# Optimization experiments

Hardware: AMD Instinct MI355X
Metric: run time of the kernel (lower is better)

## Reference

```python
import jax, jax.numpy as jnp
import numpy as np

N_NODES = 50000
N_EDGES = 600000
DIN, DH, DOUT = 128, 256, 128
BN_EPS = 1e-5
LRELU_SLOPE = 0.01


def setup_inputs() -> dict:
    key = jax.random.key(0)
    ks = jax.random.split(key, 16)
    rn = lambda k, s, sc=0.05: jax.random.normal(k, s, dtype=jnp.float32) * sc
    return {
        'nodes': jax.random.normal(ks[0], (N_NODES, DIN), dtype=jnp.float32),
        'src': jax.random.randint(ks[1], (N_EDGES,), 0, N_NODES, dtype=jnp.int32),
        'dst': jax.random.randint(ks[2], (N_EDGES,), 0, N_NODES, dtype=jnp.int32),
        # FeedForward params
        'Wf1': rn(ks[3], (DIN, DH)), 'bf1': jnp.zeros((DH,), jnp.float32),
        'gf1': jnp.ones((DH,), jnp.float32), 'bef1': jnp.zeros((DH,), jnp.float32),
        'Wf2': rn(ks[4], (DH, DIN)), 'bf2': jnp.zeros((DIN,), jnp.float32),
        'gf2': jnp.ones((DIN,), jnp.float32), 'bef2': jnp.zeros((DIN,), jnp.float32),
        # SAGEConv 1 (in->hidden)
        'Ws1': rn(ks[5], (DIN, DH)), 'Wn1': rn(ks[6], (DIN, DH)), 'b1': jnp.zeros((DH,), jnp.float32),
        'gs1': jnp.ones((DH,), jnp.float32), 'bs1': jnp.zeros((DH,), jnp.float32),
        # SAGEConv 2 (hidden->out)
        'Ws2': rn(ks[7], (DH, DOUT)), 'Wn2': rn(ks[8], (DH, DOUT)), 'b2': jnp.zeros((DOUT,), jnp.float32),
        'gs2': jnp.ones((DOUT,), jnp.float32), 'bs2': jnp.zeros((DOUT,), jnp.float32),
    }


def _bn(x, gamma, beta):
    # BatchNorm1d, training mode: batch stats over node dim, biased variance
    mu = jnp.mean(x, axis=0)
    var = jnp.mean(jnp.square(x - mu), axis=0)
    return (x - mu) * jax.lax.rsqrt(var + BN_EPS) * gamma + beta


def _sage_mean(x, src, dst, Wself, Wneigh, bias):
    # DGL SAGEConv('mean'): out = x@Wself + mean_{src->dst}(x[src])@Wneigh + bias
    n = x.shape[0]
    deg = jax.ops.segment_sum(jnp.ones_like(src, dtype=x.dtype), dst, num_segments=n)
    agg = jax.ops.segment_sum(x[src], dst, num_segments=n)  # [N, d] irregular scatter-add
    h_neigh = agg / jnp.maximum(deg, 1.0)[:, None]
    return x @ Wself + h_neigh @ Wneigh + bias


def reference(nodes, src, dst, Wf1, bf1, gf1, bef1, Wf2, bf2, gf2, bef2,
              Ws1, Wn1, b1, gs1, bs1, Ws2, Wn2, b2, gs2, bs2):
    # FeedForward (dropout=0 -> identity)
    h = jax.nn.relu(_bn(nodes @ Wf1 + bf1, gf1, bef1))
    h = jax.nn.relu(_bn(h @ Wf2 + bf2, gf2, bef2))
    # SAGE layer 1
    h1 = _sage_mean(h, src, dst, Ws1, Wn1, b1)
    h1 = jax.nn.leaky_relu(_bn(h1, gs1, bs1), LRELU_SLOPE)
    # SAGE layer 2
    h2 = _sage_mean(h1, src, dst, Ws2, Wn2, b2)
    return jax.nn.leaky_relu(_bn(h2, gs2, bs2), LRELU_SLOPE)
```

## Files before the change

### kernel.cpp

```cpp
#include <hip/hip_runtime.h>

#define DIN 128
#define BN_EPS 1e-5f

typedef __attribute__((ext_vector_type(8))) short bf16x8;
typedef __attribute__((ext_vector_type(4))) float f32x4;
typedef unsigned int u32;

__device__ __forceinline__ ushort f2bf(float f) {
    unsigned u = __float_as_uint(f);
    u += 0x7fffu + ((u >> 16) & 1u);
    return (ushort)(u >> 16);
}
__device__ __forceinline__ float bf2f(ushort h) {
    return __uint_as_float(((unsigned)h) << 16);
}

template<int KC, int STATS>
__global__ __launch_bounds__(256) void gemm_wreg(
    const ushort* __restrict__ A, const ushort* __restrict__ BT,
    ushort* __restrict__ C, int mStrips, int N, int K, int logNG,
    float* __restrict__ gsums, float* __restrict__ gsqs)
{
    int tid = threadIdx.x;
    int lane = tid & 63;
    int gw = blockIdx.x * 4 + (tid >> 6);
    int wg = gw & ((1 << logNG) - 1);
    int set = gw >> logNG;
    int totalSets = (gridDim.x * 4) >> logNG;
    int cl = lane & 15, q = lane >> 4;
    int colBase = wg * 64;

    bf16x8 bf[4][KC];
    #pragma unroll
    for (int nt = 0; nt < 4; nt++) {
        const ushort* bp = BT + (long)(colBase + nt * 16 + cl) * K + q * 8;
        #pragma unroll
        for (int kc = 0; kc < KC; kc++)
            bf[nt][kc] = *(const bf16x8*)(bp + kc * 32);
    }

    float ssum[4] = {0.f, 0.f, 0.f, 0.f};
    float ssq[4]  = {0.f, 0.f, 0.f, 0.f};

    for (int strip = set; strip < mStrips; strip += totalSets) {
        int rowBase = strip * 16;
        const ushort* ap = A + (long)(rowBase + cl) * K + q * 8;
        bf16x8 af[KC];
        #pragma unroll
        for (int kc = 0; kc < KC; kc++)
            af[kc] = *(const bf16x8*)(ap + kc * 32);
        f32x4 acc[4] = {};
        #pragma unroll
        for (int kc = 0; kc < KC; kc++)
            #pragma unroll
            for (int nt = 0; nt < 4; nt++)
                acc[nt] = __builtin_amdgcn_mfma_f32_16x16x32_bf16(af[kc], bf[nt][kc], acc[nt], 0, 0, 0);
        #pragma unroll
        for (int nt = 0; nt < 4; nt++) {
            #pragma unroll
            for (int r = 0; r < 4; r++) {
                float v = acc[nt][r];
                long row = rowBase + q * 4 + r;
                C[row * N + colBase + nt * 16 + cl] = f2bf(v);
                if (STATS) { ssum[nt] += v; ssq[nt] += v * v; }
            }
        }
    }

    if (STATS) {
        #pragma unroll
        for (int nt = 0; nt < 4; nt++) {
            ssum[nt] += __shfl_xor(ssum[nt], 16, 64);
            ssum[nt] += __shfl_xor(ssum[nt], 32, 64);
            ssq[nt]  += __shfl_xor(ssq[nt], 16, 64);
            ssq[nt]  += __shfl_xor(ssq[nt], 32, 64);
        }
        if (q == 0) {
            #pragma unroll
            for (int nt = 0; nt < 4; nt++) {
                atomicAdd(&gsums[colBase + nt * 16 + cl], ssum[nt]);
                atomicAdd(&gsqs[colBase + nt * 16 + cl], ssq[nt]);
            }
        }
    }
}

__global__ void bnparam_kernel(const float* __restrict__ sums, const float* __restrict__ sqs,
                               const float* __restrict__ gamma, const float* __restrict__ beta,
                               float* __restrict__ scale, float* __restrict__ shift,
                               int N, float invM)
{
    int c = blockIdx.x * blockDim.x + threadIdx.x;
    if (c < N) {
        float mean = sums[c] * invM;
        float var = sqs[c] * invM - mean * mean;
        float sc = gamma[c] * rsqrtf(var + BN_EPS);
        scale[c] = sc;
        shift[c] = beta[c] - mean * sc;
    }
}

__global__ __launch_bounds__(256) void bnact_bf16(
    const ushort* __restrict__ X, const float* __restrict__ scale, const float* __restrict__ shift,
    ushort* __restrict__ O, int total4, int logN, int outStride, float negSlope)
{
    int stride = gridDim.x * blockDim.x;
    int Nm1 = (1 << logN) - 1;
    for (int t = blockIdx.x * blockDim.x + threadIdx.x; t < total4; t += stride) {
        int idx = t * 4;
        int row = idx >> logN;
        int c = idx & Nm1;
        ushort4 v4 = *(const ushort4*)&X[idx];
        float4 sc = *(const float4*)&scale[c];
        float4 sh = *(const float4*)&shift[c];
        float a = bf2f(v4.x) * sc.x + sh.x; a = (a > 0.f) ? a : a * negSlope;
        float b = bf2f(v4.y) * sc.y + sh.y; b = (b > 0.f) ? b : b * negSlope;
        float d = bf2f(v4.z) * sc.z + sh.z; d = (d > 0.f) ? d : d * negSlope;
        float e = bf2f(v4.w) * sc.w + sh.w; e = (e > 0.f) ? e : e * negSlope;
        ushort4 o; o.x = f2bf(a); o.y = f2bf(b); o.z = f2bf(d); o.w = f2bf(e);
        *(ushort4*)&O[(long)row * outStride + c] = o;
    }
}

__global__ __launch_bounds__(256) void bnact_f32(
    float* __restrict__ X, const float* __restrict__ scale, const float* __restrict__ shift,
    int total4, int logN, float negSlope)
{
    int stride = gridDim.x * blockDim.x;
    int Nm1 = (1 << logN) - 1;
    for (int t = blockIdx.x * blockDim.x + threadIdx.x; t < total4; t += stride) {
        int idx = t * 4;
        int c = idx & Nm1;
        float4 v = *(const float4*)&X[idx];
        float4 sc = *(const float4*)&scale[c];
        float4 sh = *(const float4*)&shift[c];
        float a = v.x * sc.x + sh.x; a = (a > 0.f) ? a : a * negSlope;
        float b = v.y * sc.y + sh.y; b = (b > 0.f) ? b : b * negSlope;
        float d = v.z * sc.z + sh.z; d = (d > 0.f) ? d : d * negSlope;
        float e = v.w * sc.w + sh.w; e = (e > 0.f) ? e : e * negSlope;
        *(float4*)&X[idx] = make_float4(a, b, d, e);
    }
}

__global__ __launch_bounds__(256) void colstats128(
    const float* __restrict__ X, float* __restrict__ sums, float* __restrict__ sqs, int M)
{
    __shared__ float ss[128], sq[128];
    int tid = threadIdx.x;
    if (tid < 128) { ss[tid] = 0.f; sq[tid] = 0.f; }
    __syncthreads();
    int cg = tid & 31;
    int worker = (blockIdx.x << 3) | (tid >> 5);
    int totalW = gridDim.x << 3;
    float4 s4 = make_float4(0, 0, 0, 0), q4 = make_float4(0, 0, 0, 0);
    for (int r = worker; r < M; r += totalW) {
        float4 v = *(const float4*)&X[(long)r * 128 + cg * 4];
        s4.x += v.x; s4.y += v.y; s4.z += v.z; s4.w += v.w;
        q4.x += v.x * v.x; q4.y += v.y * v.y; q4.z += v.z * v.z; q4.w += v.w * v.w;
    }
    atomicAdd(&ss[cg * 4 + 0], s4.x); atomicAdd(&sq[cg * 4 + 0], q4.x);
    atomicAdd(&ss[cg * 4 + 1], s4.y); atomicAdd(&sq[cg * 4 + 1], q4.y);
    atomicAdd(&ss[cg * 4 + 2], s4.z); atomicAdd(&sq[cg * 4 + 2], q4.z);
    atomicAdd(&ss[cg * 4 + 3], s4.w); atomicAdd(&sq[cg * 4 + 3], q4.w);
    __syncthreads();
    if (tid < 128) { atomicAdd(&sums[tid], ss[tid]); atomicAdd(&sqs[tid], sq[tid]); }
}

__global__ void convert_nodes(const float* __restrict__ X, ushort* __restrict__ O, int total4)
{
    int t = blockIdx.x * blockDim.x + threadIdx.x;
    if (t < total4) {
        float4 v = *(const float4*)&X[t * 4];
        ushort4 o; o.x = f2bf(v.x); o.y = f2bf(v.y); o.z = f2bf(v.z); o.w = f2bf(v.w);
        *(ushort4*)&O[t * 4] = o;
    }
}

__global__ void wt_all(const float* __restrict__ W0, const float* __restrict__ W1,
                       const float* __restrict__ W2, const float* __restrict__ W3,
                       const float* __restrict__ W4, const float* __restrict__ W5,
                       ushort* __restrict__ WT)
{
    int seg = blockIdx.y;
    const float* W; int logK, dstBase, stride, kOff;
    switch (seg) {
        case 0: W = W0; logK = 7; dstBase = 0;      stride = 128; kOff = 0;   break;
        case 1: W = W1; logK = 8; dstBase = 32768;  stride = 256; kOff = 0;   break;
        case 2: W = W2; logK = 7; dstBase = 65536;  stride = 256; kOff = 0;   break;
        case 3: W = W3; logK = 7; dstBase = 65536;  stride = 256; kOff = 128; break;
        case 4: W = W4; logK = 8; dstBase = 131072; stride = 256; kOff = 0;   break;
        default:W = W5; logK = 8; dstBase = 163840; stride = 256; kOff = 0;   break;
    }
    int t = blockIdx.x * blockDim.x + threadIdx.x;
    int N = 32768 >> logK;
    int k = t & ((1 << logK) - 1);
    int n = t >> logK;
    WT[(long)dstBase + (long)n * stride + kOff + k] = f2bf(W[(long)k * N + n]);
}

__global__ void degcount_kernel(const int* __restrict__ dst, int* __restrict__ degi, int E)
{
    int i = blockIdx.x * blockDim.x + threadIdx.x;
    if (i < E) atomicAdd(&degi[dst[i]], 1);
}

__global__ __launch_bounds__(256) void scan_block_sums(const int* __restrict__ degi,
                                                       int* __restrict__ partial, int n)
{
    __shared__ int s[256];
    int i = blockIdx.x * 256 + threadIdx.x;
    s[threadIdx.x] = (i < n) ? degi[i] : 0;
    __syncthreads();
    for (int off = 128; off > 0; off >>= 1) {
        if (threadIdx.x < off) s[threadIdx.x] += s[threadIdx.x + off];
        __syncthreads();
    }
    if (threadIdx.x == 0) partial[blockIdx.x] = s[0];
}

__global__ __launch_bounds__(256) void scan_partials(int* __restrict__ partial, int nb)
{
    __shared__ int s[256];
    int v = (threadIdx.x < nb) ? partial[threadIdx.x] : 0;
    s[threadIdx.x] = v;
    __syncthreads();
    for (int off = 1; off < 256; off <<= 1) {
        int t = (threadIdx.x >= off) ? s[threadIdx.x - off] : 0;
        __syncthreads();
        s[threadIdx.x] += t;
        __syncthreads();
    }
    if (threadIdx.x < nb) partial[threadIdx.x] = s[threadIdx.x] - v;
}

__global__ __launch_bounds__(256) void scan_final(const int* __restrict__ degi,
                                                  const int* __restrict__ partial,
                                                  int* __restrict__ rowstart, int n)
{
    __shared__ int s[256];
    int i = blockIdx.x * 256 + threadIdx.x;
    int v = (i < n) ? degi[i] : 0;
    s[threadIdx.x] = v;
    __syncthreads();
    for (int off = 1; off < 256; off <<= 1) {
        int t = (threadIdx.x >= off) ? s[threadIdx.x - off] : 0;
        __syncthreads();
        s[threadIdx.x] += t;
        __syncthreads();
    }
    if (i < n) rowstart[i] = partial[blockIdx.x] + s[threadIdx.x] - v;
}

__global__ void fillcsr_kernel(const int* __restrict__ src, const int* __restrict__ dst,
                               const int* __restrict__ rowstart, int* __restrict__ cursor,
                               int* __restrict__ csr, int E)
{
    int i = blockIdx.x * blockDim.x + threadIdx.x;
    if (i < E) {
        int d = dst[i];
        int p = atomicAdd(&cursor[d], 1);
        csr[rowstart[d] + p] = src[i];
    }
}

__global__ __launch_bounds__(256) void gather_bf(
    const ushort* __restrict__ X, const int* __restrict__ rowstart,
    const int* __restrict__ degi, const int* __restrict__ csr,
    ushort* __restrict__ O, int nN)
{
    int wv = (blockIdx.x * blockDim.x + threadIdx.x) >> 6;
    int lane = threadIdx.x & 63;
    if (wv >= nN) return;
    int start = rowstart[wv], d = degi[wv];
    float a0 = 0.f, a1 = 0.f;
    int col = lane * 2;
    int j = 0;
    for (; j + 4 <= d; j += 4) {
        int s0 = csr[start + j + 0];
        int s1 = csr[start + j + 1];
        int s2 = csr[start + j + 2];
        int s3 = csr[start + j + 3];
        unsigned p0 = *(const unsigned*)(X + (long)s0 * 256 + col);
        unsigned p1 = *(const unsigned*)(X + (long)s1 * 256 + col);
        unsigned p2 = *(const unsigned*)(X + (long)s2 * 256 + col);
        unsigned p3 = *(const unsigned*)(X + (long)s3 * 256 + col);
        a0 += bf2f((ushort)(p0 & 0xffff)) + bf2f((ushort)(p1 & 0xffff))
            + bf2f((ushort)(p2 & 0xffff)) + bf2f((ushort)(p3 & 0xffff));
        a1 += bf2f((ushort)(p0 >> 16)) + bf2f((ushort)(p1 >> 16))
            + bf2f((ushort)(p2 >> 16)) + bf2f((ushort)(p3 >> 16));
    }
    for (; j < d; j++) {
        int s0 = csr[start + j];
        unsigned p0 = *(const unsigned*)(X + (long)s0 * 256 + col);
        a0 += bf2f((ushort)(p0 & 0xffff));
        a1 += bf2f((ushort)(p0 >> 16));
    }
    float inv = 1.f / fmaxf((float)d, 1.f);
    unsigned o = (unsigned)f2bf(a0 * inv) | ((unsigned)f2bf(a1 * inv) << 16);
    *(unsigned*)(O + (long)wv * 256 + col) = o;
}

__global__ __launch_bounds__(256) void gather_fuse(
    const ushort* __restrict__ Z, const int* __restrict__ rowstart,
    const int* __restrict__ degi, const int* __restrict__ csr,
    float* __restrict__ O, int nN)
{
    int wv = (blockIdx.x * blockDim.x + threadIdx.x) >> 6;
    int lane = threadIdx.x & 63;
    if (wv >= nN) return;
    int start = rowstart[wv], d = degi[wv];
    float a0 = 0.f, a1 = 0.f;
    int col = lane * 2;
    int j = 0;
    for (; j + 4 <= d; j += 4) {
        int s0 = csr[start + j + 0];
        int s1 = csr[start + j + 1];
        int s2 = csr[start + j + 2];
        int s3 = csr[start + j + 3];
        unsigned p0 = *(const unsigned*)(Z + (long)s0 * 256 + col);
        unsigned p1 = *(const unsigned*)(Z + (long)s1 * 256 + col);
        unsigned p2 = *(const unsigned*)(Z + (long)s2 * 256 + col);
        unsigned p3 = *(const unsigned*)(Z + (long)s3 * 256 + col);
        a0 += bf2f((ushort)(p0 & 0xffff)) + bf2f((ushort)(p1 & 0xffff))
            + bf2f((ushort)(p2 & 0xffff)) + bf2f((ushort)(p3 & 0xffff));
        a1 += bf2f((ushort)(p0 >> 16)) + bf2f((ushort)(p1 >> 16))
            + bf2f((ushort)(p2 >> 16)) + bf2f((ushort)(p3 >> 16));
    }
    for (; j < d; j++) {
        int s0 = csr[start + j];
        unsigned p0 = *(const unsigned*)(Z + (long)s0 * 256 + col);
        a0 += bf2f((ushort)(p0 & 0xffff));
        a1 += bf2f((ushort)(p0 >> 16));
    }
    float inv = 1.f / fmaxf((float)d, 1.f);
    unsigned sv = *(const unsigned*)(Z + (long)wv * 256 + 128 + col);
    float s0 = bf2f((ushort)(sv & 0xffff));
    float s1 = bf2f((ushort)(sv >> 16));
    *(float2*)(O + (long)wv * 128 + col) = make_float2(a0 * inv + s0, a1 * inv + s1);
}

extern "C" void kernel_launch(void* const* d_in, const int* in_sizes, int n_in,
                              void* d_out, int out_size, void* d_ws, size_t ws_size,
                              hipStream_t stream)
{
    const float* nodes = (const float*)d_in[0];
    const int*   src   = (const int*)d_in[1];
    const int*   dst   = (const int*)d_in[2];
    const float* Wf1   = (const float*)d_in[3];
    const float* gf1   = (const float*)d_in[5];
    const float* bef1  = (const float*)d_in[6];
    const float* Wf2   = (const float*)d_in[7];
    const float* gf2   = (const float*)d_in[9];
    const float* bef2  = (const float*)d_in[10];
    const float* Ws1   = (const float*)d_in[11];
    const float* Wn1   = (const float*)d_in[12];
    const float* gs1   = (const float*)d_in[14];
    const float* bs1   = (const float*)d_in[15];
    const float* Ws2   = (const float*)d_in[16];
    const float* Wn2   = (const float*)d_in[17];
    const float* gs2   = (const float*)d_in[19];
    const float* bs2   = (const float*)d_in[20];

    int nN = in_sizes[0] / DIN;
    int nE = in_sizes[1];
    float* out = (float*)d_out;
    int mStrips = nN / 16;

    ushort* PRE = (ushort*)d_ws;
    ushort* BF1 = PRE + (size_t)nN * 256;
    ushort* BF2 = BF1 + (size_t)nN * 256;
    float* stats = (float*)(BF2 + (size_t)nN * 256);
    float* scale = stats + 2048;
    float* shift = scale + 256;
    ushort* WT   = (ushort*)(shift + 256);
    int* degi     = (int*)(WT + 196608);
    int* cursor   = degi + nN;
    int* rowstart = cursor + nN;
    int* partial  = rowstart + nN;
    int* csr      = partial + 256;

    ushort* Wf1T = WT;
    ushort* Wf2T = WT + 32768;
    ushort* Wc1T = WT + 65536;
    ushort* Wc2T = WT + 131072;

    dim3 blk(256);
    auto cdiv = [](int a, int b) { return (a + b - 1) / b; };
    int nScanBlocks = cdiv(nN, 256);

    convert_nodes<<<dim3(cdiv(nN * DIN / 4, 256)), blk, 0, stream>>>(nodes, BF1, nN * DIN / 4);
    wt_all<<<dim3(128, 6), blk, 0, stream>>>(Wf1, Wf2, Ws1, Wn1, Wn2, Ws2, WT);
    hipMemsetAsync(stats, 0, 2048 * sizeof(float), stream);
    hipMemsetAsync(degi, 0, 2 * (size_t)nN * sizeof(int), stream);

    degcount_kernel<<<dim3(cdiv(nE, 256)), blk, 0, stream>>>(dst, degi, nE);
    scan_block_sums<<<dim3(nScanBlocks), blk, 0, stream>>>(degi, partial, nN);
    scan_partials<<<dim3(1), blk, 0, stream>>>(partial, nScanBlocks);
    scan_final<<<dim3(nScanBlocks), blk, 0, stream>>>(degi, partial, rowstart, nN);
    fillcsr_kernel<<<dim3(cdiv(nE, 256)), blk, 0, stream>>>(src, dst, rowstart, cursor, csr, nE);

    gemm_wreg<4, 1><<<dim3(512), blk, 0, stream>>>(BF1, Wf1T, PRE, mStrips, 256, 128, 2, stats, stats + 256);
    bnparam_kernel<<<dim3(1), blk, 0, stream>>>(stats, stats + 256, gf1, bef1, scale, shift, 256, 1.0f / nN);
    bnact_bf16<<<dim3(2048), blk, 0, stream>>>(PRE, scale, shift, BF1, nN * 256 / 4, 8, 256, 0.0f);

    gemm_wreg<8, 1><<<dim3(256), blk, 0, stream>>>(BF1, Wf2T, PRE, mStrips, 128, 256, 1, stats + 512, stats + 768);
    bnparam_kernel<<<dim3(1), blk, 0, stream>>>(stats + 512, stats + 768, gf2, bef2, scale, shift, 128, 1.0f / nN);
    bnact_bf16<<<dim3(2048), blk, 0, stream>>>(PRE, scale, shift, BF2, nN * 128 / 4, 7, 256, 0.0f);

    gather_bf<<<dim3(cdiv(nN * 64, 256)), blk, 0, stream>>>(BF2, rowstart, degi, csr, BF2 + 128, nN);

    gemm_wreg<8, 1><<<dim3(512), blk, 0, stream>>>(BF2, Wc1T, PRE, mStrips, 256, 256, 2, stats + 1024, stats + 1280);
    bnparam_kernel<<<dim3(1), blk, 0, stream>>>(stats + 1024, stats + 1280, gs1, bs1, scale, shift, 256, 1.0f / nN);
    bnact_bf16<<<dim3(2048), blk, 0, stream>>>(PRE, scale, shift, BF1, nN * 256 / 4, 8, 256, 0.01f);

    gemm_wreg<8, 0><<<dim3(512), blk, 0, stream>>>(BF1, Wc2T, BF2, mStrips, 256, 256, 2, nullptr, nullptr);
    gather_fuse<<<dim3(cdiv(nN * 64, 256)), blk, 0, stream>>>(BF2, rowstart, degi, csr, out, nN);

    colstats128<<<dim3(120), blk, 0, stream>>>(out, stats + 1536, stats + 1792, nN);
    bnparam_kernel<<<dim3(1), blk, 0, stream>>>(stats + 1536, stats + 1792, gs2, bs2, scale, shift, 128, 1.0f / nN);
    bnact_f32<<<dim3(2048), blk, 0, stream>>>(out, scale, shift, nN * 128 / 4, 7, 0.01f);
}
```

Measured before the change: 418.5 us.

## Fuse setup kernels, BN parameter computation, scan stages, and final column stats

Merges the input conversion, weight transposes and memsets into one setup kernel. BN scale/shift computation moves into each bnact kernel's prologue, the partial-sum scan is folded into scan_final, and the final column statistics are accumulated inside gather_fuse instead of a separate pass. bnact kernels also switch to 8-wide vector loads. The aim is to cut launch count and one full read of the output, at the cost of redundant per-block BN parameter and prefix recomputation plus more atomics.

```diff
diff --git a/kernel.cpp b/kernel.cpp
--- a/kernel.cpp
+++ b/kernel.cpp
@@ -4,8 +4,8 @@
 #define BN_EPS 1e-5f
 
 typedef __attribute__((ext_vector_type(8))) short bf16x8;
+typedef __attribute__((ext_vector_type(8))) unsigned short us8;
 typedef __attribute__((ext_vector_type(4))) float f32x4;
-typedef unsigned int u32;
 
 __device__ __forceinline__ ushort f2bf(float f) {
     unsigned u = __float_as_uint(f);
@@ -86,117 +86,128 @@
     }
 }
 
-__global__ void bnparam_kernel(const float* __restrict__ sums, const float* __restrict__ sqs,
-                               const float* __restrict__ gamma, const float* __restrict__ beta,
-                               float* __restrict__ scale, float* __restrict__ shift,
-                               int N, float invM)
-{
-    int c = blockIdx.x * blockDim.x + threadIdx.x;
-    if (c < N) {
-        float mean = sums[c] * invM;
-        float var = sqs[c] * invM - mean * mean;
-        float sc = gamma[c] * rsqrtf(var + BN_EPS);
-        scale[c] = sc;
-        shift[c] = beta[c] - mean * sc;
-    }
-}
-
+__global__ __launch_bounds__(256) void setup_all(
+    const float* __restrict__ nodes, ushort* __restrict__ Xbf, int nConv4, int nbConv,
+    const float* __restrict__ W0, const float* __restrict__ W1,
+    const float* __restrict__ W2, const float* __restrict__ W3,
+    const float* __restrict__ W4, const float* __restrict__ W5,
+    ushort* __restrict__ WT,
+    int* __restrict__ zeroInts, int nZero4, int nbZero,
+    float* __restrict__ stats)
+{
+    int b = blockIdx.x;
+    int tid = threadIdx.x;
+    if (b < nbConv) {
+        int t = b * 256 + tid;
+        if (t < nConv4) {
+            float4 v = *(const float4*)&nodes[(long)t * 4];
+            ushort4 o; o.x = f2bf(v.x); o.y = f2bf(v.y); o.z = f2bf(v.z); o.w = f2bf(v.w);
+            *(ushort4*)&Xbf[(long)t * 4] = o;
+        }
+        return;
+    }
+    b -= nbConv;
+    if (b < 768) {
+        int seg = b >> 7;
+        const float* W; int logK, dstBase, stride, kOff;
+        switch (seg) {
+            case 0: W = W0; logK = 7; dstBase = 0;      stride = 128; kOff = 0;   break;
+            case 1: W = W1; logK = 8; dstBase = 32768;  stride = 256; kOff = 0;   break;
+            case 2: W = W2; logK = 7; dstBase = 65536;  stride = 256; kOff = 0;   break;
+            case 3: W = W3; logK = 7; dstBase = 65536;  stride = 256; kOff = 128; break;
+            case 4: W = W4; logK = 8; dstBase = 131072; stride = 256; kOff = 0;   break;
+            default:W = W5; logK = 8; dstBase = 163840; stride = 256; kOff = 0;   break;
+        }
+        int t = (b & 127) * 256 + tid;
+        int N = 32768 >> logK;
+        int k = t & ((1 << logK) - 1);
+        int n = t >> logK;
+        WT[(long)dstBase + (long)n * stride + kOff + k] = f2bf(W[(long)k * N + n]);
+        return;
+    }
+    b -= 768;
+    if (b < nbZero) {
+        int t = b * 256 + tid;
+        if (t < nZero4) *(int4*)&zeroInts[(long)t * 4] = make_int4(0, 0, 0, 0);
+        return;
+    }
+    b -= nbZero;
+    int t = b * 256 + tid;
+    if (t < 512) *(float4*)&stats[(long)t * 4] = make_float4(0, 0, 0, 0);
+}
+
+template<int LOGN>
 __global__ __launch_bounds__(256) void bnact_bf16(
-    const ushort* __restrict__ X, const float* __restrict__ scale, const float* __restrict__ shift,
-    ushort* __restrict__ O, int total4, int logN, int outStride, float negSlope)
-{
-    int stride = gridDim.x * blockDim.x;
-    int Nm1 = (1 << logN) - 1;
-    for (int t = blockIdx.x * blockDim.x + threadIdx.x; t < total4; t += stride) {
-        int idx = t * 4;
-        int row = idx >> logN;
-        int c = idx & Nm1;
-        ushort4 v4 = *(const ushort4*)&X[idx];
-        float4 sc = *(const float4*)&scale[c];
-        float4 sh = *(const float4*)&shift[c];
-        float a = bf2f(v4.x) * sc.x + sh.x; a = (a > 0.f) ? a : a * negSlope;
-        float b = bf2f(v4.y) * sc.y + sh.y; b = (b > 0.f) ? b : b * negSlope;
-        float d = bf2f(v4.z) * sc.z + sh.z; d = (d > 0.f) ? d : d * negSlope;
-        float e = bf2f(v4.w) * sc.w + sh.w; e = (e > 0.f) ? e : e * negSlope;
-        ushort4 o; o.x = f2bf(a); o.y = f2bf(b); o.z = f2bf(d); o.w = f2bf(e);
-        *(ushort4*)&O[(long)row * outStride + c] = o;
+    const ushort* __restrict__ X,
+    const float* __restrict__ sums, const float* __restrict__ sqs,
+    const float* __restrict__ gamma, const float* __restrict__ beta, float invM,
+    ushort* __restrict__ O, int nRows, int outStride, float negSlope)
+{
+    constexpr int NCH = 1 << LOGN;
+    __shared__ float ssc[NCH], ssh[NCH];
+    int tid = threadIdx.x;
+    if (tid < NCH) {
+        float mean = sums[tid] * invM;
+        float var = sqs[tid] * invM - mean * mean;
+        float sc = gamma[tid] * rsqrtf(var + BN_EPS);
+        ssc[tid] = sc;
+        ssh[tid] = beta[tid] - mean * sc;
+    }
+    __syncthreads();
+    int cb = (tid * 8) & (NCH - 1);
+    float4 sA = *(const float4*)&ssc[cb];
+    float4 sB = *(const float4*)&ssc[cb + 4];
+    float4 hA = *(const float4*)&ssh[cb];
+    float4 hB = *(const float4*)&ssh[cb + 4];
+    const int rpb = (256 * 8) >> LOGN;
+    int r0 = blockIdx.x * rpb + ((tid * 8) >> LOGN);
+    int rstride = gridDim.x * rpb;
+    for (int row = r0; row < nRows; row += rstride) {
+        us8 v = *(const us8*)&X[(long)row * NCH + cb];
+        float f0 = bf2f(v[0]) * sA.x + hA.x; f0 = (f0 > 0.f) ? f0 : f0 * negSlope;
+        float f1 = bf2f(v[1]) * sA.y + hA.y; f1 = (f1 > 0.f) ? f1 : f1 * negSlope;
+        float f2 = bf2f(v[2]) * sA.z + hA.z; f2 = (f2 > 0.f) ? f2 : f2 * negSlope;
+        float f3 = bf2f(v[3]) * sA.w + hA.w; f3 = (f3 > 0.f) ? f3 : f3 * negSlope;
+        float f4 = bf2f(v[4]) * sB.x + hB.x; f4 = (f4 > 0.f) ? f4 : f4 * negSlope;
+        float f5 = bf2f(v[5]) * sB.y + hB.y; f5 = (f5 > 0.f) ? f5 : f5 * negSlope;
+        float f6 = bf2f(v[6]) * sB.z + hB.z; f6 = (f6 > 0.f) ? f6 : f6 * negSlope;
+        float f7 = bf2f(v[7]) * sB.w + hB.w; f7 = (f7 > 0.f) ? f7 : f7 * negSlope;
+        us8 o;
+        o[0] = f2bf(f0); o[1] = f2bf(f1); o[2] = f2bf(f2); o[3] = f2bf(f3);
+        o[4] = f2bf(f4); o[5] = f2bf(f5); o[6] = f2bf(f6); o[7] = f2bf(f7);
+        *(us8*)&O[(long)row * outStride + cb] = o;
     }
 }
 
 __global__ __launch_bounds__(256) void bnact_f32(
-    float* __restrict__ X, const float* __restrict__ scale, const float* __restrict__ shift,
-    int total4, int logN, float negSlope)
-{
-    int stride = gridDim.x * blockDim.x;
-    int Nm1 = (1 << logN) - 1;
-    for (int t = blockIdx.x * blockDim.x + threadIdx.x; t < total4; t += stride) {
-        int idx = t * 4;
-        int c = idx & Nm1;
-        float4 v = *(const float4*)&X[idx];
-        float4 sc = *(const float4*)&scale[c];
-        float4 sh = *(const float4*)&shift[c];
+    float* __restrict__ X,
+    const float* __restrict__ sums, const float* __restrict__ sqs,
+    const float* __restrict__ gamma, const float* __restrict__ beta, float invM,
+    int nRows, float negSlope)
+{
+    __shared__ float ssc[128], ssh[128];
+    int tid = threadIdx.x;
+    if (tid < 128) {
+        float mean = sums[tid] * invM;
+        float var = sqs[tid] * invM - mean * mean;
+        float sc = gamma[tid] * rsqrtf(var + BN_EPS);
+        ssc[tid] = sc;
+        ssh[tid] = beta[tid] - mean * sc;
+    }
+    __syncthreads();
+    int cb = (tid * 4) & 127;
+    float4 sc = *(const float4*)&ssc[cb];
+    float4 sh = *(const float4*)&ssh[cb];
+    int r0 = blockIdx.x * 8 + ((tid * 4) >> 7);
+    int rstride = gridDim.x * 8;
+    for (int row = r0; row < nRows; row += rstride) {
+        float4 v = *(const float4*)&X[(long)row * 128 + cb];
         float a = v.x * sc.x + sh.x; a = (a > 0.f) ? a : a * negSlope;
         float b = v.y * sc.y + sh.y; b = (b > 0.f) ? b : b * negSlope;
         float d = v.z * sc.z + sh.z; d = (d > 0.f) ? d : d * negSlope;
         float e = v.w * sc.w + sh.w; e = (e > 0.f) ? e : e * negSlope;
-        *(float4*)&X[idx] = make_float4(a, b, d, e);
-    }
-}
-
-__global__ __launch_bounds__(256) void colstats128(
-    const float* __restrict__ X, float* __restrict__ sums, float* __restrict__ sqs, int M)
-{
-    __shared__ float ss[128], sq[128];
-    int tid = threadIdx.x;
-    if (tid < 128) { ss[tid] = 0.f; sq[tid] = 0.f; }
-    __syncthreads();
-    int cg = tid & 31;
-    int worker = (blockIdx.x << 3) | (tid >> 5);
-    int totalW = gridDim.x << 3;
-    float4 s4 = make_float4(0, 0, 0, 0), q4 = make_float4(0, 0, 0, 0);
-    for (int r = worker; r < M; r += totalW) {
-        float4 v = *(const float4*)&X[(long)r * 128 + cg * 4];
-        s4.x += v.x; s4.y += v.y; s4.z += v.z; s4.w += v.w;
-        q4.x += v.x * v.x; q4.y += v.y * v.y; q4.z += v.z * v.z; q4.w += v.w * v.w;
-    }
-    atomicAdd(&ss[cg * 4 + 0], s4.x); atomicAdd(&sq[cg * 4 + 0], q4.x);
-    atomicAdd(&ss[cg * 4 + 1], s4.y); atomicAdd(&sq[cg * 4 + 1], q4.y);
-    atomicAdd(&ss[cg * 4 + 2], s4.z); atomicAdd(&sq[cg * 4 + 2], q4.z);
-    atomicAdd(&ss[cg * 4 + 3], s4.w); atomicAdd(&sq[cg * 4 + 3], q4.w);
-    __syncthreads();
-    if (tid < 128) { atomicAdd(&sums[tid], ss[tid]); atomicAdd(&sqs[tid], sq[tid]); }
-}
-
-__global__ void convert_nodes(const float* __restrict__ X, ushort* __restrict__ O, int total4)
-{
-    int t = blockIdx.x * blockDim.x + threadIdx.x;
-    if (t < total4) {
-        float4 v = *(const float4*)&X[t * 4];
-        ushort4 o; o.x = f2bf(v.x); o.y = f2bf(v.y); o.z = f2bf(v.z); o.w = f2bf(v.w);
-        *(ushort4*)&O[t * 4] = o;
-    }
-}
-
-__global__ void wt_all(const float* __restrict__ W0, const float* __restrict__ W1,
-                       const float* __restrict__ W2, const float* __restrict__ W3,
-                       const float* __restrict__ W4, const float* __restrict__ W5,
-                       ushort* __restrict__ WT)
-{
-    int seg = blockIdx.y;
-    const float* W; int logK, dstBase, stride, kOff;
-    switch (seg) {
-        case 0: W = W0; logK = 7; dstBase = 0;      stride = 128; kOff = 0;   break;
-        case 1: W = W1; logK = 8; dstBase = 32768;  stride = 256; kOff = 0;   break;
-        case 2: W = W2; logK = 7; dstBase = 65536;  stride = 256; kOff = 0;   break;
-        case 3: W = W3; logK = 7; dstBase = 65536;  stride = 256; kOff = 128; break;
-        case 4: W = W4; logK = 8; dstBase = 131072; stride = 256; kOff = 0;   break;
-        default:W = W5; logK = 8; dstBase = 163840; stride = 256; kOff = 0;   break;
-    }
-    int t = blockIdx.x * blockDim.x + threadIdx.x;
-    int N = 32768 >> logK;
-    int k = t & ((1 << logK) - 1);
-    int n = t >> logK;
-    WT[(long)dstBase + (long)n * stride + kOff + k] = f2bf(W[(long)k * N + n]);
+        *(float4*)&X[(long)row * 128 + cb] = make_float4(a, b, d, e);
+    }
 }
 
 __global__ void degcount_kernel(const int* __restrict__ dst, int* __restrict__ degi, int E)
@@ -219,37 +230,31 @@
     if (threadIdx.x == 0) partial[blockIdx.x] = s[0];
 }
 
-__global__ __launch_bounds__(256) void scan_partials(int* __restrict__ partial, int nb)
-{
-    __shared__ int s[256];
-    int v = (threadIdx.x < nb) ? partial[threadIdx.x] : 0;
-    s[threadIdx.x] = v;
-    __syncthreads();
-    for (int off = 1; off < 256; off <<= 1) {
-        int t = (threadIdx.x >= off) ? s[threadIdx.x - off] : 0;
-        __syncthreads();
-        s[threadIdx.x] += t;
-        __syncthreads();
-    }
-    if (threadIdx.x < nb) partial[threadIdx.x] = s[threadIdx.x] - v;
-}
-
 __global__ __launch_bounds__(256) void scan_final(const int* __restrict__ degi,
                                                   const int* __restrict__ partial,
-                                                  int* __restrict__ rowstart, int n)
+                                                  int* __restrict__ rowstart, int n, int nb)
 {
     __shared__ int s[256];
-    int i = blockIdx.x * 256 + threadIdx.x;
+    __shared__ int ps[256];
+    int tid = threadIdx.x;
+    ps[tid] = (tid < nb && tid < (int)blockIdx.x) ? partial[tid] : 0;
+    __syncthreads();
+    for (int off = 128; off > 0; off >>= 1) {
+        if (tid < off) ps[tid] += ps[tid + off];
+        __syncthreads();
+    }
+    int offset = ps[0];
+    int i = blockIdx.x * 256 + tid;
     int v = (i < n) ? degi[i] : 0;
-    s[threadIdx.x] = v;
+    s[tid] = v;
     __syncthreads();
     for (int off = 1; off < 256; off <<= 1) {
-        int t = (threadIdx.x >= off) ? s[threadIdx.x - off] : 0;
+        int t = (tid >= off) ? s[tid - off] : 0;
         __syncthreads();
-        s[threadIdx.x] += t;
+        s[tid] += t;
         __syncthreads();
     }
-    if (i < n) rowstart[i] = partial[blockIdx.x] + s[threadIdx.x] - v;
+    if (i < n) rowstart[i] = offset + s[tid] - v;
 }
 
 __global__ void fillcsr_kernel(const int* __restrict__ src, const int* __restrict__ dst,
@@ -304,40 +309,52 @@
 __global__ __launch_bounds__(256) void gather_fuse(
     const ushort* __restrict__ Z, const int* __restrict__ rowstart,
     const int* __restrict__ degi, const int* __restrict__ csr,
-    float* __restrict__ O, int nN)
-{
-    int wv = (blockIdx.x * blockDim.x + threadIdx.x) >> 6;
-    int lane = threadIdx.x & 63;
-    if (wv >= nN) return;
-    int start = rowstart[wv], d = degi[wv];
-    float a0 = 0.f, a1 = 0.f;
+    float* __restrict__ O, float* __restrict__ gsums, float* __restrict__ gsqs, int nN)
+{
+    __shared__ float ls[128], lq[128];
+    int tid = threadIdx.x;
+    if (tid < 128) { ls[tid] = 0.f; lq[tid] = 0.f; }
+    __syncthreads();
+    int lane = tid & 63;
     int col = lane * 2;
-    int j = 0;
-    for (; j + 4 <= d; j += 4) {
-        int s0 = csr[start + j + 0];
-        int s1 = csr[start + j + 1];
-        int s2 = csr[start + j + 2];
-        int s3 = csr[start + j + 3];
-        unsigned p0 = *(const unsigned*)(Z + (long)s0 * 256 + col);
-        unsigned p1 = *(const unsigned*)(Z + (long)s1 * 256 + col);
-        unsigned p2 = *(const unsigned*)(Z + (long)s2 * 256 + col);
-        unsigned p3 = *(const unsigned*)(Z + (long)s3 * 256 + col);
-        a0 += bf2f((ushort)(p0 & 0xffff)) + bf2f((ushort)(p1 & 0xffff))
-            + bf2f((ushort)(p2 & 0xffff)) + bf2f((ushort)(p3 & 0xffff));
-        a1 += bf2f((ushort)(p0 >> 16)) + bf2f((ushort)(p1 >> 16))
-            + bf2f((ushort)(p2 >> 16)) + bf2f((ushort)(p3 >> 16));
-    }
-    for (; j < d; j++) {
-        int s0 = csr[start + j];
-        unsigned p0 = *(const unsigned*)(Z + (long)s0 * 256 + col);
-        a0 += bf2f((ushort)(p0 & 0xffff));
-        a1 += bf2f((ushort)(p0 >> 16));
-    }
-    float inv = 1.f / fmaxf((float)d, 1.f);
-    unsigned sv = *(const unsigned*)(Z + (long)wv * 256 + 128 + col);
-    float s0 = bf2f((ushort)(sv & 0xffff));
-    float s1 = bf2f((ushort)(sv >> 16));
-    *(float2*)(O + (long)wv * 128 + col) = make_float2(a0 * inv + s0, a1 * inv + s1);
+    float sum0 = 0.f, sq0 = 0.f, sum1 = 0.f, sq1 = 0.f;
+    int wstride = gridDim.x * 4;
+    for (int wv = blockIdx.x * 4 + (tid >> 6); wv < nN; wv += wstride) {
+        int start = rowstart[wv], d = degi[wv];
+        float a0 = 0.f, a1 = 0.f;
+        int j = 0;
+        for (; j + 4 <= d; j += 4) {
+            int s0 = csr[start + j + 0];
+            int s1 = csr[start + j + 1];
+            int s2 = csr[start + j + 2];
+            int s3 = csr[start + j + 3];
+            unsigned p0 = *(const unsigned*)(Z + (long)s0 * 256 + col);
+            unsigned p1 = *(const unsigned*)(Z + (long)s1 * 256 + col);
+            unsigned p2 = *(const unsigned*)(Z + (long)s2 * 256 + col);
+            unsigned p3 = *(const unsigned*)(Z + (long)s3 * 256 + col);
+            a0 += bf2f((ushort)(p0 & 0xffff)) + bf2f((ushort)(p1 & 0xffff))
+                + bf2f((ushort)(p2 & 0xffff)) + bf2f((ushort)(p3 & 0xffff));
+            a1 += bf2f((ushort)(p0 >> 16)) + bf2f((ushort)(p1 >> 16))
+                + bf2f((ushort)(p2 >> 16)) + bf2f((ushort)(p3 >> 16));
+        }
+        for (; j < d; j++) {
+            int s0 = csr[start + j];
+            unsigned p0 = *(const unsigned*)(Z + (long)s0 * 256 + col);
+            a0 += bf2f((ushort)(p0 & 0xffff));
+            a1 += bf2f((ushort)(p0 >> 16));
+        }
+        float inv = 1.f / fmaxf((float)d, 1.f);
+        unsigned sv = *(const unsigned*)(Z + (long)wv * 256 + 128 + col);
+        float r0 = a0 * inv + bf2f((ushort)(sv & 0xffff));
+        float r1 = a1 * inv + bf2f((ushort)(sv >> 16));
+        *(float2*)(O + (long)wv * 128 + col) = make_float2(r0, r1);
+        sum0 += r0; sq0 += r0 * r0;
+        sum1 += r1; sq1 += r1 * r1;
+    }
+    atomicAdd(&ls[col], sum0);     atomicAdd(&lq[col], sq0);
+    atomicAdd(&ls[col + 1], sum1); atomicAdd(&lq[col + 1], sq1);
+    __syncthreads();
+    if (tid < 128) { atomicAdd(&gsums[tid], ls[tid]); atomicAdd(&gsqs[tid], lq[tid]); }
 }
 
 extern "C" void kernel_launch(void* const* d_in, const int* in_sizes, int n_in,
@@ -366,6 +383,7 @@
     int nE = in_sizes[1];
     float* out = (float*)d_out;
     int mStrips = nN / 16;
+    float invM = 1.0f / nN;
 
     ushort* PRE = (ushort*)d_ws;
     ushort* BF1 = PRE + (size_t)nN * 256;
@@ -389,35 +407,38 @@
     auto cdiv = [](int a, int b) { return (a + b - 1) / b; };
     int nScanBlocks = cdiv(nN, 256);
 
-    convert_nodes<<<dim3(cdiv(nN * DIN / 4, 256)), blk, 0, stream>>>(nodes, BF1, nN * DIN / 4);
-    wt_all<<<dim3(128, 6), blk, 0, stream>>>(Wf1, Wf2, Ws1, Wn1, Wn2, Ws2, WT);
-    hipMemsetAsync(stats, 0, 2048 * sizeof(float), stream);
-    hipMemsetAsync(degi, 0, 2 * (size_t)nN * sizeof(int), stream);
+    int nConv4 = nN * DIN / 4;
+    int nbConv = cdiv(nConv4, 256);
+    int nZero4 = (2 * nN) / 4;
+    int nbZero = cdiv(nZero4, 256);
+    setup_all<<<dim3(nbConv + 768 + nbZero + 2), blk, 0, stream>>>(
+        nodes, BF1, nConv4, nbConv,
+        Wf1, Wf2, Ws1, Wn1, Wn2, Ws2, WT,
+        degi, nZero4, nbZero, stats);
 
     degcount_kernel<<<dim3(cdiv(nE, 256)), blk, 0, stream>>>(dst, degi, nE);
     scan_block_sums<<<dim3(nScanBlocks), blk, 0, stream>>>(degi, partial, nN);
-    scan_partials<<<dim3(1), blk, 0, stream>>>(partial, nScanBlocks);
-    scan_final<<<dim3(nScanBlocks), blk, 0, stream>>>(degi, partial, rowstart, nN);
+    scan_final<<<dim3(nScanBlocks), blk, 0, stream>>>(degi, partial, rowstart, nN, nScanBlocks);
     fillcsr_kernel<<<dim3(cdiv(nE, 256)), blk, 0, stream>>>(src, dst, rowstart, cursor, csr, nE);
 
     gemm_wreg<4, 1><<<dim3(512), blk, 0, stream>>>(BF1, Wf1T, PRE, mStrips, 256, 128, 2, stats, stats + 256);
-    bnparam_kernel<<<dim3(1), blk, 0, stream>>>(stats, stats + 256, gf1, bef1, scale, shift, 256, 1.0f / nN);
-    bnact_bf16<<<dim3(2048), blk, 0, stream>>>(PRE, scale, shift, BF1, nN * 256 / 4, 8, 256, 0.0f);
+    bnact_bf16<8><<<dim3(2048), blk, 0, stream>>>(PRE, stats, stats + 256, gf1, bef1, invM,
+                                                  BF1, nN, 256, 0.0f);
 
     gemm_wreg<8, 1><<<dim3(256), blk, 0, stream>>>(BF1, Wf2T, PRE, mStrips, 128, 256, 1, stats + 512, stats + 768);
-    bnparam_kernel<<<dim3(1), blk, 0, stream>>>(stats + 512, stats + 768, gf2, bef2, scale, shift, 128, 1.0f / nN);
-    bnact_bf16<<<dim3(2048), blk, 0, stream>>>(PRE, scale, shift, BF2, nN * 128 / 4, 7, 256, 0.0f);
+    bnact_bf16<7><<<dim3(2048), blk, 0, stream>>>(PRE, stats + 512, stats + 768, gf2, bef2, invM,
+                                                  BF2, nN, 256, 0.0f);
 
     gather_bf<<<dim3(cdiv(nN * 64, 256)), blk, 0, stream>>>(BF2, rowstart, degi, csr, BF2 + 128, nN);
 
     gemm_wreg<8, 1><<<dim3(512), blk, 0, stream>>>(BF2, Wc1T, PRE, mStrips, 256, 256, 2, stats + 1024, stats + 1280);
-    bnparam_kernel<<<dim3(1), blk, 0, stream>>>(stats + 1024, stats + 1280, gs1, bs1, scale, shift, 256, 1.0f / nN);
-    bnact_bf16<<<dim3(2048), blk, 0, stream>>>(PRE, scale, shift, BF1, nN * 256 / 4, 8, 256, 0.01f);
+    bnact_bf16<8><<<dim3(2048), blk, 0, stream>>>(PRE, stats + 1024, stats + 1280, gs1, bs1, invM,
+                                                  BF1, nN, 256, 0.01f);
 
     gemm_wreg<8, 0><<<dim3(512), blk, 0, stream>>>(BF1, Wc2T, BF2, mStrips, 256, 256, 2, nullptr, nullptr);
-    gather_fuse<<<dim3(cdiv(nN * 64, 256)), blk, 0, stream>>>(BF2, rowstart, degi, csr, out, nN);
-
-    colstats128<<<dim3(120), blk, 0, stream>>>(out, stats + 1536, stats + 1792, nN);
-    bnparam_kernel<<<dim3(1), blk, 0, stream>>>(stats + 1536, stats + 1792, gs2, bs2, scale, shift, 128, 1.0f / nN);
-    bnact_f32<<<dim3(2048), blk, 0, stream>>>(out, scale, shift, nN * 128 / 4, 7, 0.01f);
-}
+    gather_fuse<<<dim3(2048), blk, 0, stream>>>(BF2, rowstart, degi, csr, out,
+                                                stats + 1536, stats + 1792, nN);
+
+    bnact_f32<<<dim3(2048), blk, 0, stream>>>(out, stats + 1536, stats + 1792, gs2, bs2, invM,
+                                              nN, 0.01f);
+}
```

Result: slower. 430.7 us (+2.9%).
